# Kernel tuning notes

Hardware: AMD Instinct MI355X
Metric: run time of the kernel (lower is better)

Reference implementation:

```python
import jax, jax.numpy as jnp
import numpy as np

DEPTH = 8
HID = 512
EXP = 4
EPS = 1e-5


def setup_inputs() -> dict:
    key = jax.random.key(0)
    ks = jax.random.split(key, 12)
    B = 131072
    x = jax.random.normal(ks[0], (B, HID), dtype=jnp.float32)
    # input projection (input_dim=HID -> hidden_dim=HID)
    W_in = jax.random.normal(ks[1], (HID, HID), dtype=jnp.float32) * (1.0 / HID)
    b_in = jnp.zeros((HID,), dtype=jnp.float32)
    # stacked per-block params [DEPTH, ...]
    ln_g = jnp.ones((DEPTH, HID), dtype=jnp.float32)
    ln_b = jnp.zeros((DEPTH, HID), dtype=jnp.float32)
    W1 = jax.random.normal(ks[2], (DEPTH, HID, EXP), dtype=jnp.float32) * (1.0 / EXP)
    b1 = jnp.zeros((DEPTH, EXP), dtype=jnp.float32)
    W2 = jax.random.normal(ks[3], (DEPTH, EXP, HID), dtype=jnp.float32) * (1.0 / HID)
    b2 = jnp.zeros((DEPTH, HID), dtype=jnp.float32)
    # head (hidden_dim -> output_dim=HID)
    W_head = jax.random.normal(ks[4], (HID, HID), dtype=jnp.float32) * (1.0 / HID)
    b_head = jnp.zeros((HID,), dtype=jnp.float32)
    return {"x": x, "W_in": W_in, "b_in": b_in, "ln_g": ln_g, "ln_b": ln_b,
            "W1": W1, "b1": b1, "W2": W2, "b2": b2,
            "W_head": W_head, "b_head": b_head}


def _layernorm(x, g, b):
    mu = jnp.mean(x, axis=-1, keepdims=True)
    var = jnp.mean(jnp.square(x - mu), axis=-1, keepdims=True)
    return (x - mu) * jax.lax.rsqrt(var + EPS) * g + b


def reference(x, W_in, b_in, ln_g, ln_b, W1, b1, W2, b2, W_head, b_head):
    # mlp_input: Linear + relu (dropout=0.0 -> identity)
    h = jax.nn.relu(x @ W_in + b_in)  # [B, HID]

    def block(h, p):
        g, bb, w1, bb1, w2, bb2 = p
        z = _layernorm(h, g, bb)
        z = jax.nn.relu(z @ w1 + bb1)  # [B, EXP]
        z = z @ w2 + bb2               # [B, HID]
        return h + z, None

    h, _ = jax.lax.scan(block, h, (ln_g, ln_b, W1, b1, W2, b2))
    return h @ W_head + b_head
```

## Files before the change

kernel.cpp:

```cpp
#include <hip/hip_runtime.h>
#include <cstdint>

typedef unsigned short u16;
typedef unsigned int   u32;
typedef float  f32x4  __attribute__((ext_vector_type(4)));
typedef short  short8 __attribute__((ext_vector_type(8)));

__device__ inline float bf2f(u16 b){ u32 u=((u32)b)<<16; float f; __builtin_memcpy(&f,&u,4); return f; }
__device__ inline u16 f2bf(float f){ u32 u; __builtin_memcpy(&u,&f,4); u32 r=u+0x7FFFu+((u>>16)&1u); return (u16)(r>>16); }
__device__ inline u32 pk(float hi, float lo){ u32 a,b; __builtin_memcpy(&a,&hi,4); __builtin_memcpy(&b,&lo,4); return __builtin_amdgcn_perm(a,b,0x07060302u); }
__device__ inline u32 pkr(float hi, float lo){ return (u32)f2bf(lo) | ((u32)f2bf(hi)<<16); }
__device__ inline void gload_lds16(const void* g, void* l){
  __builtin_amdgcn_global_load_lds((const __attribute__((address_space(1))) unsigned int*)g,
                                   (__attribute__((address_space(3))) unsigned int*)l, 16, 0, 0);
}

#define CBAR(K) do{ asm volatile("s_waitcnt vmcnt(" #K ") lgkmcnt(0)" ::: "memory"); \
  __builtin_amdgcn_s_barrier(); __builtin_amdgcn_sched_barrier(0); }while(0)

__global__ __launch_bounds__(256) void prep_k(
    const float* __restrict__ W_in, const float* __restrict__ W_head,
    const float* __restrict__ ln_g, const float* __restrict__ W1,
    const float* __restrict__ W2, const float* __restrict__ b2,
    u16* __restrict__ Wt_in3, u16* __restrict__ Wt_hd3,
    u16* __restrict__ gw1f, u16* __restrict__ updA)
{
  int idx = blockIdx.x * 256 + threadIdx.x;
  if (idx < 524288){
    int which = idx >> 18;
    int q = idx & 262143;
    int t = q >> 14, o = q & 16383;
    int line = o >> 6, w = o & 63, slot = w >> 3, i = w & 7;
    int c8 = slot ^ (line & 7);
    int n = 2 * line + (c8 >> 2);
    int g = c8 & 3;
    if (which == 0){
      int k = t * 32 + g * 8 + i;
      Wt_in3[q] = f2bf(W_in[k * 512 + n]);
    } else {
      int k = t * 32 + (i < 4 ? 4 * g + i : 12 + 4 * g + i);
      Wt_hd3[q] = f2bf(W_head[k * 512 + n]);
    }
  } else if (idx < 544768){
    int q = idx - 524288;
    int d = q / 2560, r = q % 2560;
    int c = r / 160, r2 = r % 160;
    int g = r2 / 40, r3 = r2 % 40;
    int col = r3 >> 3, i = r3 & 7;
    int k = 32 * c + (i < 4 ? 4 * g + i : 12 + 4 * g + i);
    u16 v;
    if (col == 4) v = 0x3F80u;
    else          v = f2bf(ln_g[d * 512 + k] * W1[(d * 512 + k) * 4 + col]);
    gw1f[q] = v;
  } else if (idx < 577536){
    int q = idx - 544768;
    int d = q >> 12, r = q & 4095;
    int t = r >> 7, r2 = r & 127;
    int m = r2 >> 3, sl = r2 & 7;
    int k = 16 * t + m;
    u16 v = 0;
    if (sl < 4)       v = f2bf(W2[(d * 4 + sl) * 512 + k]);
    else if (sl == 4) v = f2bf(b2[d * 512 + k]);
    updA[q] = v;
  }
}

__global__ __launch_bounds__(64) void uv_k(
    const float* __restrict__ ln_g, const float* __restrict__ ln_b,
    const float* __restrict__ W1, const float* __restrict__ b1,
    float* __restrict__ U, float* __restrict__ V)
{
  int d = blockIdx.x >> 2, e = blockIdx.x & 3;
  int lane = threadIdx.x;
  float u = 0.f, v = 0.f;
  for (int k = lane; k < 512; k += 64){
    float w = W1[(d * 512 + k) * 4 + e];
    u += bf2f(f2bf(ln_g[d * 512 + k] * w));
    v += ln_b[d * 512 + k] * w;
  }
  for (int m = 1; m < 64; m <<= 1){ u += __shfl_xor(u, m); v += __shfl_xor(v, m); }
  if (lane == 0){ U[d * 4 + e] = u; V[d * 4 + e] = v + b1[d * 4 + e]; }
}

__global__ __launch_bounds__(512, 2) void fused_k(
    const float* __restrict__ x, const u16* __restrict__ Wt_in3,
    const float* __restrict__ b_in, const u16* __restrict__ Wt_hd3,
    const float* __restrict__ b_head, const u16* __restrict__ gw1f,
    const u16* __restrict__ updA, const float* __restrict__ U,
    const float* __restrict__ V, float* __restrict__ out)
{
  __shared__ __align__(16) char LT[131344];
  constexpr int SSo = 65536, ZBo = 77824;
  constexpr int MIDB = 98304, HXo = 98304;
  constexpr int UVo = 131072, SZo = 131328;
  float* sSf = (float*)(LT + SSo);
  float* zbf = (float*)(LT + ZBo);
  float* sUV = (float*)(LT + UVo);
  u16*   sZ  = (u16*)(LT + SZo);

  const int tid  = threadIdx.x;
  const int wv   = tid >> 6;
  const int lane = tid & 63;
  const int m    = lane & 15;
  const int g    = lane >> 4;
  const int nq   = wv & 3;
  const int rh   = wv >> 2;
  const size_t rowbase = (size_t)blockIdx.x * 128 + rh * 64;

  if (tid < 32) sUV[tid] = U[tid];
  else if (tid < 64) sUV[tid] = V[tid - 32];
  if (tid >= 64 && tid < 72) sZ[tid - 64] = 0;

  auto stageA = [&](const u16* W, int t, char* dst){
    const char* src = (const char*)(W + t * 16384) + tid * 16;
    char* d2 = dst + tid * 16;
    #pragma unroll
    for (int j = 0; j < 4; ++j)
      gload_lds16(src + j * 8192, d2 + j * 8192);
  };
  auto stageM = [&](int d, int bf2){
    char* dsg = LT + MIDB + bf2 * 16384;
    if (tid < 320)
      gload_lds16((const char*)gw1f + d * 5120 + tid * 16, dsg + tid * 16);
    gload_lds16((const char*)updA + d * 8192 + tid * 16, dsg + 5120 + tid * 16);
  };

  auto mkfrag = [&](f32x4 a, f32x4 b)->short8{
    union{u32 u[4]; short8 s;} t;
    t.u[0]=pkr(a[1],a[0]); t.u[1]=pkr(a[3],a[2]);
    t.u[2]=pkr(b[1],b[0]); t.u[3]=pkr(b[3],b[2]);
    return t.s;
  };
  auto mkfragT = [&](f32x4 a, f32x4 b)->short8{
    union{u32 u[4]; short8 s;} t;
    t.u[0]=pk(a[1],a[0]); t.u[1]=pk(a[3],a[2]);
    t.u[2]=pk(b[1],b[0]); t.u[3]=pk(b[3],b[2]);
    return t.s;
  };

  const int afoff = (m >> 1) * 128 + (((((m & 1) << 2) | g) ^ ((m >> 1) & 7)) << 4);

  f32x4 hv[4][4][2];
  #pragma unroll
  for (int q = 0; q < 4; ++q)
    #pragma unroll
    for (int c2 = 0; c2 < 4; ++c2){ hv[q][c2][0] = (f32x4)0.f; hv[q][c2][1] = (f32x4)0.f; }

  const float* xbase = x + (rowbase + m) * 512 + g * 8;
  f32x4 xA[4][2], xB[4][2];
  #pragma unroll
  for (int q = 0; q < 4; ++q){
    xA[q][0] = *(const f32x4*)(xbase + q * 8192);
    xA[q][1] = *(const f32x4*)(xbase + q * 8192 + 4);
    xB[q][0] = *(const f32x4*)(xbase + q * 8192 + 32);
    xB[q][1] = *(const f32x4*)(xbase + q * 8192 + 36);
  }
  stageA(Wt_in3, 0, LT);
  stageA(Wt_in3, 1, LT + 32768);
  __syncthreads();

  #pragma unroll
  for (int t = 0; t < 16; ++t){
    if (t < 14) stageA(Wt_in3, t + 2, LT + ((t + 2) % 3) * 32768);
    short8 bq[4];
    #pragma unroll
    for (int q = 0; q < 4; ++q)
      bq[q] = (t & 1) ? mkfrag(xB[q][0], xB[q][1]) : mkfrag(xA[q][0], xA[q][1]);
    if (t < 14){
      #pragma unroll
      for (int q = 0; q < 4; ++q){
        if (t & 1){
          xB[q][0] = *(const f32x4*)(xbase + q * 8192 + (t + 2) * 32);
          xB[q][1] = *(const f32x4*)(xbase + q * 8192 + (t + 2) * 32 + 4);
        } else {
          xA[q][0] = *(const f32x4*)(xbase + q * 8192 + (t + 2) * 32);
          xA[q][1] = *(const f32x4*)(xbase + q * 8192 + (t + 2) * 32 + 4);
        }
      }
    }
    const char* wb = LT + (t % 3) * 32768 + nq * 8192 + afoff;
    #pragma unroll
    for (int f = 0; f < 8; ++f){
      short8 aw = *(const short8*)(wb + f * 1024);
      #pragma unroll
      for (int q = 0; q < 4; ++q)
        hv[q][f >> 1][f & 1] =
          __builtin_amdgcn_mfma_f32_16x16x32_bf16(aw, bq[q], hv[q][f >> 1][f & 1], 0, 0, 0);
    }
    if (t < 14)       CBAR(20);
    else if (t == 14) CBAR(8);
  }

  #pragma unroll
  for (int q = 0; q < 4; ++q)
    #pragma unroll
    for (int c2 = 0; c2 < 4; ++c2)
      #pragma unroll
      for (int hf = 0; hf < 2; ++hf){
        f32x4 bi = *(const f32x4*)(b_in + nq * 128 + c2 * 32 + hf * 16 + g * 4);
        #pragma unroll
        for (int r = 0; r < 4; ++r){
          float v = hv[q][c2][hf][r] + bi[r];
          v = v > 0.f ? v : 0.f;
          hv[q][c2][hf][r] = bf2f(f2bf(v));
        }
      }

  stageM(0, 0);
  __syncthreads();
  int buf = 0;
  #pragma unroll 1
  for (int d = 0; d < 8; ++d){
    if (d < 7) stageM(d + 1, buf ^ 1);
    else       stageA(Wt_hd3, 0, LT);

    const u16* sGp = (const u16*)(LT + MIDB + buf * 16384);
    const u16* sAp = sGp + 2560;

    const u16* gb = (m < 5) ? (sGp + nq * 640 + g * 40 + m * 8) : sZ;
    const int gstep = (m < 5) ? 160 : 0;
    f32x4 aS[4], aG[4];
    #pragma unroll
    for (int q = 0; q < 4; ++q){ aS[q] = (f32x4)0.f; aG[q] = (f32x4)0.f; }
    #pragma unroll
    for (int c2 = 0; c2 < 4; ++c2){
      short8 bf = *(const short8*)(gb + c2 * gstep);
      #pragma unroll
      for (int q = 0; q < 4; ++q){
        short8 af = mkfragT(hv[q][c2][0], hv[q][c2][1]);
        aS[q] = __builtin_amdgcn_mfma_f32_16x16x32_bf16(af, bf, aS[q], 0, 0, 0);
        aG[q] = __builtin_amdgcn_mfma_f32_16x16x32_bf16(af, af, aG[q], 0, 0, 0);
      }
    }

    #pragma unroll
    for (int q = 0; q < 4; ++q){
      if (m < 5)
        *(f32x4*)(sSf + (((rh * 4 + q) * 4 + nq) * 6 + m) * 16 + 4 * g) = aS[q];
      if ((m >> 2) == g)
        sSf[(((rh * 4 + q) * 4 + nq) * 6 + 5) * 16 + m] = aG[q][m & 3];
    }
    __syncthreads();

    if (tid < 128){
      int rh2 = tid >> 6, rl = tid & 63, q2 = rl >> 4, b = rl & 15;
      float S0 = 0.f, S1 = 0.f, S2 = 0.f, S3 = 0.f, sm = 0.f, sq = 0.f;
      #pragma unroll
      for (int nn = 0; nn < 4; ++nn){
        const float* pp = sSf + (((rh2 * 4 + q2) * 4 + nn) * 6) * 16 + b;
        S0 += pp[0]; S1 += pp[16]; S2 += pp[32]; S3 += pp[48];
        sm += pp[64]; sq += pp[80];
      }
      float mu  = sm * (1.f / 512.f);
      float var = sq * (1.f / 512.f) - mu * mu;
      float rs  = rsqrtf(var + 1e-5f);
      f32x4 zz;
      float z0 = fmaf(rs, S0 - mu * sUV[d * 4 + 0], sUV[32 + d * 4 + 0]);
      float z1 = fmaf(rs, S1 - mu * sUV[d * 4 + 1], sUV[32 + d * 4 + 1]);
      float z2 = fmaf(rs, S2 - mu * sUV[d * 4 + 2], sUV[32 + d * 4 + 2]);
      float z3 = fmaf(rs, S3 - mu * sUV[d * 4 + 3], sUV[32 + d * 4 + 3]);
      zz[0] = z0 > 0.f ? z0 : 0.f;
      zz[1] = z1 > 0.f ? z1 : 0.f;
      zz[2] = z2 > 0.f ? z2 : 0.f;
      zz[3] = z3 > 0.f ? z3 : 0.f;
      *(f32x4*)(zbf + tid * 4) = zz;
    }
    __syncthreads();

    #pragma unroll
    for (int q = 0; q < 4; ++q){
      f32x4 z4 = *(const f32x4*)(zbf + (rh * 64 + q * 16 + m) * 4);
      union{u32 u[4]; short8 s;} bz;
      bz.u[0] = (g == 0) ? pk(z4[1], z4[0]) : 0u;
      bz.u[1] = (g == 0) ? pk(z4[3], z4[2]) : 0u;
      bz.u[2] = (g == 0) ? 0x00003F80u : 0u;
      bz.u[3] = 0u;
      const u16* ab = (g == 0) ? (sAp + nq * 1024 + m * 8) : sZ;
      const int ainc = (g == 0) ? 128 : 0;
      #pragma unroll
      for (int t2 = 0; t2 < 8; ++t2){
        short8 aw = *(const short8*)(ab + t2 * ainc);
        hv[q][t2 >> 1][t2 & 1] =
          __builtin_amdgcn_mfma_f32_16x16x32_bf16(aw, bz.s, hv[q][t2 >> 1][t2 & 1], 0, 0, 0);
      }
    }
    __syncthreads();
    buf ^= 1;
  }

  short8 p[4][4];
  #pragma unroll
  for (int q = 0; q < 4; ++q)
    #pragma unroll
    for (int c2 = 0; c2 < 4; ++c2)
      p[q][c2] = mkfrag(hv[q][c2][0], hv[q][c2][1]);

  f32x4 acc[4][8];
  #pragma unroll
  for (int q = 0; q < 4; ++q)
    #pragma unroll
    for (int of = 0; of < 8; ++of) acc[q][of] = (f32x4)0.f;

  if (nq == 0){
    #pragma unroll
    for (int q = 0; q < 4; ++q)
      *(short8*)(LT + HXo + rh * 4096 + (q * 64 + m * 4 + g) * 16) = p[q][0];
  }
  stageA(Wt_hd3, 1, LT + 32768);
  __syncthreads();

  #pragma unroll
  for (int c = 0; c < 16; ++c){
    if (c < 14) stageA(Wt_hd3, c + 2, LT + ((c + 2) % 3) * 32768);
    if (c < 15 && nq == ((c + 1) >> 2)){
      #pragma unroll
      for (int q = 0; q < 4; ++q)
        *(short8*)(LT + HXo + ((c + 1) & 1) * 8192 + rh * 4096 + (q * 64 + m * 4 + g) * 16)
          = p[q][(c + 1) & 3];
    }
    const char* hxb = LT + HXo + (c & 1) * 8192 + rh * 4096 + (m * 4 + g) * 16;
    short8 bh[4];
    #pragma unroll
    for (int q = 0; q < 4; ++q) bh[q] = *(const short8*)(hxb + q * 1024);
    const char* wb = LT + (c % 3) * 32768 + nq * 8192 + afoff;
    #pragma unroll
    for (int of = 0; of < 8; ++of){
      short8 aw = *(const short8*)(wb + of * 1024);
      #pragma unroll
      for (int q = 0; q < 4; ++q)
        acc[q][of] = __builtin_amdgcn_mfma_f32_16x16x32_bf16(aw, bh[q], acc[q][of], 0, 0, 0);
    }
    if (c < 14)       CBAR(4);
    else if (c == 14) CBAR(0);
  }

  #pragma unroll
  for (int q = 0; q < 4; ++q)
    #pragma unroll
    for (int of = 0; of < 8; ++of){
      f32x4 bhd = *(const f32x4*)(b_head + nq * 128 + of * 16 + g * 4);
      f32x4 v;
      #pragma unroll
      for (int r = 0; r < 4; ++r) v[r] = acc[q][of][r] + bhd[r];
      *(f32x4*)(out + (rowbase + q * 16 + m) * 512 + nq * 128 + of * 16 + g * 4) = v;
    }
}

extern "C" void kernel_launch(void* const* d_in, const int* in_sizes, int n_in,
                              void* d_out, int out_size, void* d_ws, size_t ws_size,
                              hipStream_t stream)
{
  const float* x      = (const float*)d_in[0];
  const float* W_in   = (const float*)d_in[1];
  const float* b_in   = (const float*)d_in[2];
  const float* ln_g   = (const float*)d_in[3];
  const float* ln_b   = (const float*)d_in[4];
  const float* W1     = (const float*)d_in[5];
  const float* b1     = (const float*)d_in[6];
  const float* W2     = (const float*)d_in[7];
  const float* b2     = (const float*)d_in[8];
  const float* W_head = (const float*)d_in[9];
  const float* b_head = (const float*)d_in[10];
  float* out = (float*)d_out;
  const int B = in_sizes[0] / 512;

  char* ws = (char*)d_ws;
  u16*   Wt_in3 = (u16*)ws;
  u16*   Wt_hd3 = Wt_in3 + 262144;
  u16*   gw1f   = Wt_hd3 + 262144;
  u16*   updA   = gw1f + 20480;
  float* Up     = (float*)(updA + 32768);
  float* Vp     = Up + 32;

  prep_k<<<2256, 256, 0, stream>>>(W_in, W_head, ln_g, W1, W2, b2, Wt_in3, Wt_hd3, gw1f, updA);
  uv_k<<<32, 64, 0, stream>>>(ln_g, ln_b, W1, b1, Up, Vp);
  fused_k<<<B / 128, 512, 0, stream>>>(x, Wt_in3, b_in, Wt_hd3, b_head, gw1f, updA, Up, Vp, out);
}
```

Measured before the change: 365.0 us.

## Triple-buffer block params with partial vmcnt barriers; use hardware bf16 pack

The per-block LayerNorm/MLP parameter staging goes from double to triple buffering, prefetching two blocks ahead. Full __syncthreads barriers become CBAR waits that leave some global->LDS loads in flight, and the head weight tiles are prefetched during the last two blocks. Software bf16 rounding is replaced by v_cvt_pk_bf16_f32. This adds 16KB of LDS, which may lower occupancy under the 2-blocks-per-CU launch bound, and the vmcnt counts must match the number of outstanding loads for the data to be correct.

```diff
diff --git a/kernel.cpp b/kernel.cpp
--- a/kernel.cpp
+++ b/kernel.cpp
@@ -8,8 +8,9 @@
 
 __device__ inline float bf2f(u16 b){ u32 u=((u32)b)<<16; float f; __builtin_memcpy(&f,&u,4); return f; }
 __device__ inline u16 f2bf(float f){ u32 u; __builtin_memcpy(&u,&f,4); u32 r=u+0x7FFFu+((u>>16)&1u); return (u16)(r>>16); }
+__device__ inline float ubits(u32 u){ float f; __builtin_memcpy(&f,&u,4); return f; }
 __device__ inline u32 pk(float hi, float lo){ u32 a,b; __builtin_memcpy(&a,&hi,4); __builtin_memcpy(&b,&lo,4); return __builtin_amdgcn_perm(a,b,0x07060302u); }
-__device__ inline u32 pkr(float hi, float lo){ return (u32)f2bf(lo) | ((u32)f2bf(hi)<<16); }
+__device__ inline u32 cvtpk(float lo, float hi){ u32 r; asm("v_cvt_pk_bf16_f32 %0, %1, %2" : "=v"(r) : "v"(lo), "v"(hi)); return r; }
 __device__ inline void gload_lds16(const void* g, void* l){
   __builtin_amdgcn_global_load_lds((const __attribute__((address_space(1))) unsigned int*)g,
                                    (__attribute__((address_space(3))) unsigned int*)l, 16, 0, 0);
@@ -89,10 +90,10 @@
     const u16* __restrict__ updA, const float* __restrict__ U,
     const float* __restrict__ V, float* __restrict__ out)
 {
-  __shared__ __align__(16) char LT[131344];
+  __shared__ __align__(16) char LT[147728];
   constexpr int SSo = 65536, ZBo = 77824;
   constexpr int MIDB = 98304, HXo = 98304;
-  constexpr int UVo = 131072, SZo = 131328;
+  constexpr int UVo = 147456, SZo = 147712;
   float* sSf = (float*)(LT + SSo);
   float* zbf = (float*)(LT + ZBo);
   float* sUV = (float*)(LT + UVo);
@@ -118,8 +119,8 @@
     for (int j = 0; j < 4; ++j)
       gload_lds16(src + j * 8192, d2 + j * 8192);
   };
-  auto stageM = [&](int d, int bf2){
-    char* dsg = LT + MIDB + bf2 * 16384;
+  auto stageM = [&](int d, int bf3){
+    char* dsg = LT + MIDB + bf3 * 16384;
     if (tid < 320)
       gload_lds16((const char*)gw1f + d * 5120 + tid * 16, dsg + tid * 16);
     gload_lds16((const char*)updA + d * 8192 + tid * 16, dsg + 5120 + tid * 16);
@@ -127,8 +128,8 @@
 
   auto mkfrag = [&](f32x4 a, f32x4 b)->short8{
     union{u32 u[4]; short8 s;} t;
-    t.u[0]=pkr(a[1],a[0]); t.u[1]=pkr(a[3],a[2]);
-    t.u[2]=pkr(b[1],b[0]); t.u[3]=pkr(b[3],b[2]);
+    t.u[0]=cvtpk(a[0],a[1]); t.u[1]=cvtpk(a[2],a[3]);
+    t.u[2]=cvtpk(b[0],b[1]); t.u[3]=cvtpk(b[2],b[3]);
     return t.s;
   };
   auto mkfragT = [&](f32x4 a, f32x4 b)->short8{
@@ -198,23 +199,27 @@
       #pragma unroll
       for (int hf = 0; hf < 2; ++hf){
         f32x4 bi = *(const f32x4*)(b_in + nq * 128 + c2 * 32 + hf * 16 + g * 4);
+        f32x4 v;
         #pragma unroll
-        for (int r = 0; r < 4; ++r){
-          float v = hv[q][c2][hf][r] + bi[r];
-          v = v > 0.f ? v : 0.f;
-          hv[q][c2][hf][r] = bf2f(f2bf(v));
-        }
+        for (int r = 0; r < 4; ++r){ float w = hv[q][c2][hf][r] + bi[r]; v[r] = w > 0.f ? w : 0.f; }
+        u32 ua = cvtpk(v[0], v[1]), ub = cvtpk(v[2], v[3]);
+        hv[q][c2][hf][0] = ubits(ua << 16);
+        hv[q][c2][hf][1] = ubits(ua & 0xFFFF0000u);
+        hv[q][c2][hf][2] = ubits(ub << 16);
+        hv[q][c2][hf][3] = ubits(ub & 0xFFFF0000u);
       }
 
   stageM(0, 0);
+  stageM(1, 1);
   __syncthreads();
-  int buf = 0;
+
   #pragma unroll 1
   for (int d = 0; d < 8; ++d){
-    if (d < 7) stageM(d + 1, buf ^ 1);
-    else       stageA(Wt_hd3, 0, LT);
-
-    const u16* sGp = (const u16*)(LT + MIDB + buf * 16384);
+    if (d < 6)       stageM(d + 2, (d + 2) % 3);
+    else if (d == 6) stageA(Wt_hd3, 0, LT);
+    else             stageA(Wt_hd3, 1, LT + 32768);
+
+    const u16* sGp = (const u16*)(LT + MIDB + (d % 3) * 16384);
     const u16* sAp = sGp + 2560;
 
     const u16* gb = (m < 5) ? (sGp + nq * 640 + g * 40 + m * 8) : sZ;
@@ -240,7 +245,7 @@
       if ((m >> 2) == g)
         sSf[(((rh * 4 + q) * 4 + nq) * 6 + 5) * 16 + m] = aG[q][m & 3];
     }
-    __syncthreads();
+    CBAR(8);
 
     if (tid < 128){
       int rh2 = tid >> 6, rl = tid & 63, q2 = rl >> 4, b = rl & 15;
@@ -265,7 +270,7 @@
       zz[3] = z3 > 0.f ? z3 : 0.f;
       *(f32x4*)(zbf + tid * 4) = zz;
     }
-    __syncthreads();
+    CBAR(8);
 
     #pragma unroll
     for (int q = 0; q < 4; ++q){
@@ -284,8 +289,7 @@
           __builtin_amdgcn_mfma_f32_16x16x32_bf16(aw, bz.s, hv[q][t2 >> 1][t2 & 1], 0, 0, 0);
       }
     }
-    __syncthreads();
-    buf ^= 1;
+    CBAR(1);
   }
 
   short8 p[4][4];
@@ -306,8 +310,7 @@
     for (int q = 0; q < 4; ++q)
       *(short8*)(LT + HXo + rh * 4096 + (q * 64 + m * 4 + g) * 16) = p[q][0];
   }
-  stageA(Wt_hd3, 1, LT + 32768);
-  __syncthreads();
+  CBAR(8);
 
   #pragma unroll
   for (int c = 0; c < 16; ++c){
```

New measurement: 338.2 us. 1.08x faster.
